# Kernel tuning notes

Measured on AMD Instinct MI355X. Metric: run time of the kernel, lower is better.

## Reference

```python
import jax, jax.numpy as jnp
import numpy as np

B, C, H, W = 2, 256, 64, 64
NUM_HEADS = 4
HEAD_DIM = C // NUM_HEADS
N = H * W


def setup_inputs() -> dict:
    key = jax.random.key(0)
    ks = jax.random.split(key, 10)
    x = jax.random.normal(ks[0], (B, C, H, W), dtype=jnp.float32)
    # mostly-True mask; diagonal forced True so every row has a valid key
    m = jax.random.uniform(ks[1], (B, N, N)) > 0.1
    spatial_mask = m | jnp.eye(N, dtype=bool)[None]
    s = 1.0 / np.sqrt(C)
    wq = jax.random.normal(ks[2], (C, C), dtype=jnp.float32) * s
    bq = jnp.zeros((C,), jnp.float32)
    wk = jax.random.normal(ks[3], (C, C), dtype=jnp.float32) * s
    bk = jnp.zeros((C,), jnp.float32)
    wv = jax.random.normal(ks[4], (C, C), dtype=jnp.float32) * s
    bv = jnp.zeros((C,), jnp.float32)
    # torch zero-inits out_proj; use random weights for a non-trivial baseline
    wo = jax.random.normal(ks[5], (C, C), dtype=jnp.float32) * s
    bo = jnp.zeros((C,), jnp.float32)
    return {"x": x, "spatial_mask": spatial_mask, "wq": wq, "bq": bq,
            "wk": wk, "bk": bk, "wv": wv, "bv": bv, "wo": wo, "bo": bo}


def reference(x, spatial_mask, wq, bq, wk, bk, wv, bv, wo, bo):
    b, c, h, w = x.shape
    n = h * w
    nh, hd = NUM_HEADS, HEAD_DIM
    scale = hd ** -0.5
    x_flat = x.reshape(b, c, n).transpose(0, 2, 1)           # [b, n, c]
    q = (x_flat @ wq.T + bq).reshape(b, n, nh, hd).transpose(0, 2, 1, 3)
    k = (x_flat @ wk.T + bk).reshape(b, n, nh, hd).transpose(0, 2, 1, 3)
    v = (x_flat @ wv.T + bv).reshape(b, n, nh, hd).transpose(0, 2, 1, 3)
    logits = jnp.einsum('bhqd,bhkd->bhqk', q, k) * scale      # [b, nh, n, n]
    logits = jnp.where(spatial_mask[:, None], logits, -jnp.inf)
    attn = jax.nn.softmax(logits, axis=-1)                    # dropout = identity (eval)
    out = jnp.einsum('bhqk,bhkd->bhqd', attn, v)              # [b, nh, n, hd]
    out = out.transpose(0, 2, 1, 3).reshape(b, n, c)
    out = out @ wo.T + bo
    return out.transpose(0, 2, 1).reshape(b, c, h, w)
```

## Files before the change

kernel.cpp:

```cpp
#include <hip/hip_runtime.h>
#include <math.h>

namespace {
constexpr int B_    = 2;
constexpr int C_    = 256;
constexpr int NHEAD = 4;
constexpr int HDIM  = 64;
constexpr int NTOK  = 4096;
constexpr float SCALE = 0.125f;
constexpr float LOG2E = 1.44269504f;
constexpr int QKV_BLOCKS = 3 * B_ * (NTOK / 64);
}

typedef _Float16 half8  __attribute__((ext_vector_type(8)));
typedef _Float16 half4  __attribute__((ext_vector_type(4)));
typedef __fp16   fp16x2 __attribute__((ext_vector_type(2)));
typedef float    floatx4 __attribute__((ext_vector_type(4)));
typedef int      int4v   __attribute__((ext_vector_type(4)));
typedef unsigned int uint2v __attribute__((ext_vector_type(2)));

__device__ __forceinline__ void plswap32(int &a, int &b) {
#if __has_builtin(__builtin_amdgcn_permlane32_swap)
    const uint2v r = __builtin_amdgcn_permlane32_swap((unsigned)a, (unsigned)b, false, false);
    a = (int)r[0]; b = (int)r[1];
#else
    asm volatile("s_nop 1\n\tv_permlane32_swap_b32 %0, %1\n\ts_nop 1"
                 : "+v"(a), "+v"(b));
#endif
}
__device__ __forceinline__ void plswap16(int &a, int &b) {
#if __has_builtin(__builtin_amdgcn_permlane16_swap)
    const uint2v r = __builtin_amdgcn_permlane16_swap((unsigned)a, (unsigned)b, false, false);
    a = (int)r[0]; b = (int)r[1];
#else
    asm volatile("s_nop 1\n\tv_permlane16_swap_b32 %0, %1\n\ts_nop 1"
                 : "+v"(a), "+v"(b));
#endif
}

__device__ __forceinline__ void gload_lds16(const _Float16* g, _Float16* l, int lane) {
#if __has_builtin(__builtin_amdgcn_global_load_lds)
    __builtin_amdgcn_global_load_lds(
        (const __attribute__((address_space(1))) void*)g,
        (__attribute__((address_space(3))) void*)l, 16, 0, 0);
#else
    *(half8*)((char*)l + lane * 16) = *(const half8*)g;
#endif
}

__device__ __forceinline__ half8 ldcvt8(const float* p) {
    const float4 a = *(const float4*)p;
    const float4 b = *(const float4*)(p + 4);
    half8 h;
    h[0]=(_Float16)a.x; h[1]=(_Float16)a.y; h[2]=(_Float16)a.z; h[3]=(_Float16)a.w;
    h[4]=(_Float16)b.x; h[5]=(_Float16)b.y; h[6]=(_Float16)b.z; h[7]=(_Float16)b.w;
    return h;
}

__global__ __launch_bounds__(256) void qkv_pack(
    const float* __restrict__ x,
    const float* __restrict__ wq, const float* __restrict__ wk,
    const float* __restrict__ wv,
    const float* __restrict__ bq, const float* __restrict__ bk,
    const float* __restrict__ bv,
    const unsigned int* __restrict__ m32, unsigned int* __restrict__ packed,
    _Float16* __restrict__ qo, _Float16* __restrict__ ko,
    _Float16* __restrict__ vo)
{
    if (blockIdx.x >= QKV_BLOCKS) {
        int c0 = 0, c1 = 0, c2 = 0, c3 = 0;
        #pragma unroll
        for (int i = 0; i < 16; i++) {
            const unsigned int d = m32[i];
            c0 += (d == 0x00000001u);
            c1 += (d == 0x3F803F80u);
            c2 += (d == 0x3F800000u);
            c3 += (d == 0x01010101u);
        }
        int fmt = 1, best = c1;
        if (c0 > best) { best = c0; fmt = 0; }
        if (c2 > best) { best = c2; fmt = 2; }
        if (c3 > best) { best = c3; fmt = 3; }

        const unsigned int W = (blockIdx.x - QKV_BLOCKS) * 256 + threadIdx.x;
        unsigned int bits = 0;
        if (fmt == 1) {
            const uint4* p4 = (const uint4*)(m32 + (size_t)W * 16);
            #pragma unroll
            for (int i = 0; i < 4; i++) {
                const uint4 v = p4[i];
                const unsigned int d[4] = { v.x, v.y, v.z, v.w };
                #pragma unroll
                for (int j = 0; j < 4; j++) {
                    const int e = i * 8 + j * 2;
                    bits |= ((d[j] & 0xFFFFu) ? 1u : 0u) << e;
                    bits |= ((d[j] >> 16)     ? 1u : 0u) << (e + 1);
                }
            }
        } else if (fmt != 3) {
            const uint4* p4 = (const uint4*)(m32 + (size_t)W * 32);
            #pragma unroll
            for (int i = 0; i < 8; i++) {
                const uint4 v = p4[i];
                bits |= (v.x ? 1u : 0u) << (i * 4 + 0);
                bits |= (v.y ? 1u : 0u) << (i * 4 + 1);
                bits |= (v.z ? 1u : 0u) << (i * 4 + 2);
                bits |= (v.w ? 1u : 0u) << (i * 4 + 3);
            }
        } else {
            const uint4* p4 = (const uint4*)(m32 + (size_t)W * 8);
            #pragma unroll
            for (int i = 0; i < 2; i++) {
                const uint4 v = p4[i];
                const unsigned int d[4] = { v.x, v.y, v.z, v.w };
                #pragma unroll
                for (int j = 0; j < 4; j++) {
                    const int e = (i * 4 + j) * 4;
                    bits |= ((d[j] & 0x000000FFu) ? 1u : 0u) << (e + 0);
                    bits |= ((d[j] & 0x0000FF00u) ? 1u : 0u) << (e + 1);
                    bits |= ((d[j] & 0x00FF0000u) ? 1u : 0u) << (e + 2);
                    bits |= ((d[j] & 0xFF000000u) ? 1u : 0u) << (e + 3);
                }
            }
        }
        packed[W] = bits;
        return;
    }

    const int bid = blockIdx.x;
    const int p   = bid >> 7;
    const int b   = (bid >> 6) & 1;
    const int nt  = bid & 63;

    const float* w    = (p == 0) ? wq : (p == 1) ? wk : wv;
    const float* bias = (p == 0) ? bq : (p == 1) ? bk : bv;

    const int t    = threadIdx.x;
    const int wid  = t >> 6;
    const int lane = t & 63;
    const int quad = lane >> 4;
    const int l15  = lane & 15;
    const int n0   = nt * 64;

    __shared__ _Float16 xsh[64 * 264];
    __shared__ _Float16 tbuf[64 * 72];

    const int srow = t >> 2;
    const int sc   = (t & 3) * 16;

    {
        const int cr = t >> 4;
        const int nu = (t & 15) * 4;
        const float* xb = x + (size_t)b * C_ * NTOK;
        #pragma unroll
        for (int cc = 0; cc < 16; cc++) {
            const int cl = cc * 16 + cr;
            const float4 v = *(const float4*)&xb[(size_t)cl * NTOK + n0 + nu];
            xsh[(nu + 0) * 264 + cl] = (_Float16)v.x;
            xsh[(nu + 1) * 264 + cl] = (_Float16)v.y;
            xsh[(nu + 2) * 264 + cl] = (_Float16)v.z;
            xsh[(nu + 3) * 264 + cl] = (_Float16)v.w;
        }
    }
    __syncthreads();

    const float* wrow = &w[(size_t)(wid * 16 + l15) * C_];

    for (int h = 0; h < NHEAD; h++) {
        const int co0 = h * 64;
        floatx4 acc[4];
        #pragma unroll
        for (int i = 0; i < 4; i++) acc[i] = (floatx4)0.f;

        #pragma unroll
        for (int c0 = 0; c0 < C_; c0 += 64) {
            const half8 a0 = ldcvt8(&wrow[(size_t)co0 * C_ + c0 + quad * 8]);
            const half8 a1 = ldcvt8(&wrow[(size_t)co0 * C_ + c0 + 32 + quad * 8]);
            #pragma unroll
            for (int nt2 = 0; nt2 < 4; nt2++) {
                const half8 b0 = *(const half8*)&xsh[(nt2 * 16 + l15) * 264 + c0 + quad * 8];
                const half8 b1 = *(const half8*)&xsh[(nt2 * 16 + l15) * 264 + c0 + 32 + quad * 8];
                acc[nt2] = __builtin_amdgcn_mfma_f32_16x16x32_f16(a0, b0, acc[nt2], 0, 0, 0);
                acc[nt2] = __builtin_amdgcn_mfma_f32_16x16x32_f16(a1, b1, acc[nt2], 0, 0, 0);
            }
        }

        const float4 bb4 = *(const float4*)&bias[co0 + wid * 16 + quad * 4];
        const float bb[4] = { bb4.x, bb4.y, bb4.z, bb4.w };

        if (p < 2) {
            const float osc = (p == 0) ? (SCALE * LOG2E) : 1.0f;
            #pragma unroll
            for (int nt2 = 0; nt2 < 4; nt2++) {
                half4 hv;
                #pragma unroll
                for (int i = 0; i < 4; i++)
                    hv[i] = (_Float16)((acc[nt2][i] + bb[i]) * osc);
                *(half4*)&tbuf[(nt2 * 16 + l15) * 72 + wid * 16 + quad * 4] = hv;
            }
            __syncthreads();
            _Float16* dh = (p == 0 ? qo : ko) + (size_t)(b * NHEAD + h) * NTOK * HDIM;
            const half8 o0 = *(const half8*)&tbuf[srow * 72 + sc];
            const half8 o1 = *(const half8*)&tbuf[srow * 72 + sc + 8];
            *(half8*)&dh[(size_t)(n0 + srow) * HDIM + sc]     = o0;
            *(half8*)&dh[(size_t)(n0 + srow) * HDIM + sc + 8] = o1;
        } else {
            #pragma unroll
            for (int nt2 = 0; nt2 < 4; nt2++)
                #pragma unroll
                for (int i = 0; i < 4; i++)
                    tbuf[(wid * 16 + quad * 4 + i) * 72 + nt2 * 16 + l15] =
                        (_Float16)(acc[nt2][i] + bb[i]);
            __syncthreads();
            _Float16* vth = vo + (size_t)(b * NHEAD + h) * HDIM * NTOK;
            const half8 o0 = *(const half8*)&tbuf[srow * 72 + sc];
            const half8 o1 = *(const half8*)&tbuf[srow * 72 + sc + 8];
            *(half8*)&vth[(size_t)srow * NTOK + n0 + sc]     = o0;
            *(half8*)&vth[(size_t)srow * NTOK + n0 + sc + 8] = o1;
        }
        __syncthreads();
    }
}

__global__ __launch_bounds__(512) void attn(
    const _Float16* __restrict__ q, const _Float16* __restrict__ k,
    const _Float16* __restrict__ vt, const unsigned int* __restrict__ mpacked,
    _Float16* __restrict__ ao)
{
    const int b  = blockIdx.z;
    const int h  = blockIdx.y;
    const int q0 = blockIdx.x * 128;
    const int t    = threadIdx.x;
    const int w    = t >> 6;
    const int lane = t & 63;
    const int quad = lane >> 4;
    const int l15  = lane & 15;
    const int half = w >> 2;
    const int w4   = w & 3;
    const int koff = half * (NTOK / 2);

    __shared__ __align__(16) char smem_raw[65536];
    _Float16* const sbase = (_Float16*)(smem_raw + half * 32768);

    const size_t head_off = (size_t)(b * NHEAD + h) * NTOK * HDIM;
    const _Float16* qb  = q  + head_off;
    const _Float16* kb  = k  + head_off;
    const _Float16* vtb = vt + head_off;
    const unsigned int* mrow = mpacked + (size_t)b * NTOK * 128;

    const int qrowa = q0 + w4 * 16 + l15;
    const int qrowb = qrowa + 64;
    const half8 aq0a = *(const half8*)&qb[(size_t)qrowa * HDIM + quad * 8];
    const half8 aq1a = *(const half8*)&qb[(size_t)qrowa * HDIM + 32 + quad * 8];
    const half8 aq0b = *(const half8*)&qb[(size_t)qrowb * HDIM + quad * 8];
    const half8 aq1b = *(const half8*)&qb[(size_t)qrowb * HDIM + 32 + quad * 8];
    const unsigned int* mqa = &mrow[(size_t)qrowa * 128];
    const unsigned int* mqb = &mrow[(size_t)qrowb * 128];

    const int jr  = l15 & 7;
    const int xs0 = (quad ^ jr) << 3;
    const int xs1 = ((quad + 4) ^ jr) << 3;

    uint2 mwa = *(const uint2*)&mqa[koff >> 5];
    uint2 mwb = *(const uint2*)&mqb[koff >> 5];
    uint2 mwa_nxt = mwa, mwb_nxt = mwb;

    float l_a = 0.f, l_b = 0.f;
    floatx4 oacca[4], oaccb[4];
    #pragma unroll
    for (int i = 0; i < 4; i++) { oacca[i] = (floatx4)0.f; oaccb[i] = (floatx4)0.f; }

#define STAGE(WO, K0N)                                                        \
    {                                                                         \
        const int rl = lane >> 3;                       \
        const int xc = ((lane & 7) ^ rl) << 3;        \
        const int c0 = w4 * 2, c1 = c0 + 1;                                   \
        gload_lds16(&kb[(size_t)((K0N) + c0 * 8 + rl) * HDIM + xc],           \
                    &sbase[(WO) + c0 * 512], lane);                           \
        gload_lds16(&kb[(size_t)((K0N) + c1 * 8 + rl) * HDIM + xc],           \
                    &sbase[(WO) + c1 * 512], lane);                           \
        gload_lds16(&vtb[(size_t)(c0 * 8 + rl) * NTOK + (K0N) + xc],          \
                    &sbase[(WO) + 4096 + c0 * 512], lane);                    \
        gload_lds16(&vtb[(size_t)(c1 * 8 + rl) * NTOK + (K0N) + xc],          \
                    &sbase[(WO) + 4096 + c1 * 512], lane);                    \
    }

    STAGE(0, koff)
    __syncthreads();

#define SOFTMAX_CT(SA, CT, WORD, SH, LL, Pa, Pb)                                  \
    {                                                                             \
        const unsigned nib = ((WORD) >> ((SH) + quad * 4)) & 0xFu;                \
        const float p0 = __builtin_amdgcn_exp2f((nib & 1u) ? SA[CT][0] : -3.0e38f);\
        const float p1 = __builtin_amdgcn_exp2f((nib & 2u) ? SA[CT][1] : -3.0e38f);\
        const float p2 = __builtin_amdgcn_exp2f((nib & 4u) ? SA[CT][2] : -3.0e38f);\
        const float p3 = __builtin_amdgcn_exp2f((nib & 8u) ? SA[CT][3] : -3.0e38f);\
        LL += (p0 + p1) + (p2 + p3);                                              \
        Pa = __builtin_bit_cast(int, __builtin_amdgcn_cvt_pkrtz(p0, p1));         \
        Pb = __builtin_bit_cast(int, __builtin_amdgcn_cvt_pkrtz(p2, p3));         \
    }

#define ATTN_TILE(RO, WO, KT, PF)                                                 \
    {                                                                             \
        if (PF) {                                                                 \
            const int k0n = koff + (KT) * 64 + 64;                                \
            STAGE(WO, k0n)                                                        \
            mwa_nxt = *(const uint2*)&mqa[k0n >> 5];                              \
            mwb_nxt = *(const uint2*)&mqb[k0n >> 5];                              \
        }                                                                         \
        floatx4 saa[4], sab[4];                                                   \
        __builtin_amdgcn_s_setprio(1);                                            \
        _Pragma("unroll")                                                         \
        for (int ct = 0; ct < 4; ct++) {                                          \
            saa[ct] = (floatx4)0.f; sab[ct] = (floatx4)0.f;                       \
            const half8 ka0 = *(const half8*)&sbase[(RO) + (ct*16 + l15)*64 + xs0];\
            const half8 ka1 = *(const half8*)&sbase[(RO) + (ct*16 + l15)*64 + xs1];\
            saa[ct] = __builtin_amdgcn_mfma_f32_16x16x32_f16(ka0, aq0a, saa[ct], 0, 0, 0); \
            saa[ct] = __builtin_amdgcn_mfma_f32_16x16x32_f16(ka1, aq1a, saa[ct], 0, 0, 0); \
            sab[ct] = __builtin_amdgcn_mfma_f32_16x16x32_f16(ka0, aq0b, sab[ct], 0, 0, 0); \
            sab[ct] = __builtin_amdgcn_mfma_f32_16x16x32_f16(ka1, aq1b, sab[ct], 0, 0, 0); \
        }                                                                         \
        __builtin_amdgcn_s_setprio(0);                                            \
        int A00,A01,A10,A11,A20,A21,A30,A31;                                      \
        int B00,B01,B10,B11,B20,B21,B30,B31;                                      \
        SOFTMAX_CT(saa, 0, mwa.x, 0,  l_a, A00, A01)                              \
        SOFTMAX_CT(saa, 1, mwa.x, 16, l_a, A10, A11)                              \
        SOFTMAX_CT(saa, 2, mwa.y, 0,  l_a, A20, A21)                              \
        SOFTMAX_CT(saa, 3, mwa.y, 16, l_a, A30, A31)                              \
        SOFTMAX_CT(sab, 0, mwb.x, 0,  l_b, B00, B01)                              \
        SOFTMAX_CT(sab, 1, mwb.x, 16, l_b, B10, B11)                              \
        SOFTMAX_CT(sab, 2, mwb.y, 0,  l_b, B20, B21)                              \
        SOFTMAX_CT(sab, 3, mwb.y, 16, l_b, B30, B31)                              \
        mwa = mwa_nxt; mwb = mwb_nxt;                                             \
        plswap32(A00, A10); plswap32(A01, A11);                                   \
        plswap32(A20, A30); plswap32(A21, A31);                                   \
        plswap16(A00, A10); plswap16(A01, A11);                                   \
        plswap16(A20, A30); plswap16(A21, A31);                                   \
        plswap32(B00, B10); plswap32(B01, B11);                                   \
        plswap32(B20, B30); plswap32(B21, B31);                                   \
        plswap16(B00, B10); plswap16(B01, B11);                                   \
        plswap16(B20, B30); plswap16(B21, B31);                                   \
        const half8 pb0a = __builtin_bit_cast(half8, (int4v){A00, A01, A10, A11});\
        const half8 pb1a = __builtin_bit_cast(half8, (int4v){A20, A21, A30, A31});\
        const half8 pb0b = __builtin_bit_cast(half8, (int4v){B00, B01, B10, B11});\
        const half8 pb1b = __builtin_bit_cast(half8, (int4v){B20, B21, B30, B31});\
        __builtin_amdgcn_s_setprio(1);                                            \
        _Pragma("unroll")                                                         \
        for (int dt = 0; dt < 4; dt++) {                                          \
            const half8 va0 = *(const half8*)&sbase[(RO) + 4096 + (dt*16 + l15)*64 + xs0];\
            const half8 va1 = *(const half8*)&sbase[(RO) + 4096 + (dt*16 + l15)*64 + xs1];\
            oacca[dt] = __builtin_amdgcn_mfma_f32_16x16x32_f16(va0, pb0a, oacca[dt], 0, 0, 0); \
            oacca[dt] = __builtin_amdgcn_mfma_f32_16x16x32_f16(va1, pb1a, oacca[dt], 0, 0, 0); \
            oaccb[dt] = __builtin_amdgcn_mfma_f32_16x16x32_f16(va0, pb0b, oaccb[dt], 0, 0, 0); \
            oaccb[dt] = __builtin_amdgcn_mfma_f32_16x16x32_f16(va1, pb1b, oaccb[dt], 0, 0, 0); \
        }                                                                         \
        __builtin_amdgcn_s_setprio(0);                                            \
        __syncthreads();                                                          \
    }

    for (int kt2 = 0; kt2 < 15; kt2++) {
        ATTN_TILE(0,    8192, 2 * kt2,     1)
        ATTN_TILE(8192, 0,    2 * kt2 + 1, 1)
    }
    ATTN_TILE(0,    8192, 30, 1)
    ATTN_TILE(8192, 0,    31, 0)

#undef ATTN_TILE
#undef SOFTMAX_CT
#undef STAGE

    l_a += __shfl_xor(l_a, 16, 64);
    l_a += __shfl_xor(l_a, 32, 64);
    l_b += __shfl_xor(l_b, 16, 64);
    l_b += __shfl_xor(l_b, 32, 64);

    __syncthreads();
    float* oex = (float*)smem_raw;
    float* lex = (float*)(smem_raw + 32768);
    if (w >= 4) {
        float* dst = &oex[((size_t)(w - 4) * 64 + lane) * 32];
        #pragma unroll
        for (int dt = 0; dt < 4; dt++) {
            *(floatx4*)&dst[dt * 4]      = oacca[dt];
            *(floatx4*)&dst[16 + dt * 4] = oaccb[dt];
        }
        if (quad == 0) {
            lex[(w - 4) * 16 + l15]      = l_a;
            lex[64 + (w - 4) * 16 + l15] = l_b;
        }
    }
    __syncthreads();
    if (w < 4) {
        const float* src = &oex[((size_t)w * 64 + lane) * 32];
        const float lta = l_a + lex[w * 16 + l15];
        const float ltb = l_b + lex[64 + w * 16 + l15];
        const float inva = (lta > 0.f) ? (1.0f / lta) : 0.f;
        const float invb = (ltb > 0.f) ? (1.0f / ltb) : 0.f;
        _Float16* aoba = ao + ((size_t)b * NTOK + q0 + w * 16 + l15) * C_ + h * 64;
        _Float16* aobb = ao + ((size_t)b * NTOK + q0 + 64 + w * 16 + l15) * C_ + h * 64;
        #pragma unroll
        for (int dt = 0; dt < 4; dt++) {
            const floatx4 o2a = *(const floatx4*)&src[dt * 4];
            const floatx4 o2b = *(const floatx4*)&src[16 + dt * 4];
            half4 ra, rb;
            #pragma unroll
            for (int rr = 0; rr < 4; rr++) {
                ra[rr] = (_Float16)((oacca[dt][rr] + o2a[rr]) * inva);
                rb[rr] = (_Float16)((oaccb[dt][rr] + o2b[rr]) * invb);
            }
            *(half4*)&aoba[dt * 16 + quad * 4] = ra;
            *(half4*)&aobb[dt * 16 + quad * 4] = rb;
        }
    }
}

__global__ __launch_bounds__(256) void out_mfma(
    const _Float16* __restrict__ ao, const float* __restrict__ wo,
    const float* __restrict__ bo, float* __restrict__ out)
{
    const int nt  = blockIdx.x;
    const int cot = blockIdx.y;
    const int b   = blockIdx.z;
    const int t    = threadIdx.x;
    const int wid  = t >> 6;
    const int lane = t & 63;
    const int quad = lane >> 4;
    const int l15  = lane & 15;
    const int n0  = nt * 64;
    const int co0 = cot * 64;

    __shared__ float tf[64 * 68];

    floatx4 acc[4];
    #pragma unroll
    for (int i = 0; i < 4; i++) acc[i] = (floatx4)0.f;

    const float* wrow = &wo[(size_t)(co0 + wid * 16 + l15) * C_];
    const _Float16* aob  = ao + ((size_t)b * NTOK + n0) * C_;

    #pragma unroll
    for (int c0 = 0; c0 < C_; c0 += 64) {
        const half8 a0 = ldcvt8(&wrow[c0 + quad * 8]);
        const half8 a1 = ldcvt8(&wrow[c0 + 32 + quad * 8]);
        #pragma unroll
        for (int nt2 = 0; nt2 < 4; nt2++) {
            const half8 b0 = *(const half8*)&aob[(size_t)(nt2 * 16 + l15) * C_ + c0 + quad * 8];
            const half8 b1 = *(const half8*)&aob[(size_t)(nt2 * 16 + l15) * C_ + c0 + 32 + quad * 8];
            acc[nt2] = __builtin_amdgcn_mfma_f32_16x16x32_f16(a0, b0, acc[nt2], 0, 0, 0);
            acc[nt2] = __builtin_amdgcn_mfma_f32_16x16x32_f16(a1, b1, acc[nt2], 0, 0, 0);
        }
    }

    #pragma unroll
    for (int nt2 = 0; nt2 < 4; nt2++)
        #pragma unroll
        for (int i = 0; i < 4; i++)
            tf[(wid * 16 + quad * 4 + i) * 68 + nt2 * 16 + l15] = acc[nt2][i];
    __syncthreads();

    const int row = t >> 2;
    const int c4  = (t & 3) * 16;
    const float bb = bo[co0 + row];
    float* orow = &out[((size_t)(b * C_ + co0 + row)) * NTOK + n0 + c4];
    #pragma unroll
    for (int u = 0; u < 4; u++) {
        float4 v = *(const float4*)&tf[row * 68 + c4 + u * 4];
        v.x += bb; v.y += bb; v.z += bb; v.w += bb;
        *(float4*)&orow[u * 4] = v;
    }
}

extern "C" void kernel_launch(void* const* d_in, const int* in_sizes, int n_in,
                              void* d_out, int out_size, void* d_ws, size_t ws_size,
                              hipStream_t stream) {
    const float* x    = (const float*)d_in[0];
    const void*  mask = d_in[1];
    const float* wq   = (const float*)d_in[2];
    const float* bq   = (const float*)d_in[3];
    const float* wk   = (const float*)d_in[4];
    const float* bk   = (const float*)d_in[5];
    const float* wv   = (const float*)d_in[6];
    const float* bv   = (const float*)d_in[7];
    const float* wo   = (const float*)d_in[8];
    const float* bo   = (const float*)d_in[9];
    float* out = (float*)d_out;

    const size_t qkv_elems = (size_t)B_ * NHEAD * NTOK * HDIM;
    _Float16* wsh = (_Float16*)d_ws;
    _Float16* qbuf  = wsh;
    _Float16* kbuf  = wsh + qkv_elems;
    _Float16* vtbuf = wsh + 2 * qkv_elems;
    _Float16* aobuf = wsh + 3 * qkv_elems;
    unsigned int* mpacked = (unsigned int*)(wsh + 4 * qkv_elems);

    qkv_pack<<<dim3(QKV_BLOCKS + (B_ * NTOK * 128) / 256), 256, 0, stream>>>(
        x, wq, wk, wv, bq, bk, bv,
        (const unsigned int*)mask, mpacked, qbuf, kbuf, vtbuf);
    attn<<<dim3(NTOK / 128, NHEAD, B_), 512, 0, stream>>>(
        qbuf, kbuf, vtbuf, mpacked, aobuf);
    out_mfma<<<dim3(NTOK / 64, C_ / 64, B_), 256, 0, stream>>>(
        aobuf, wo, bo, out);
}
```

Before: 284.2 us.

## Triple-buffer K/V tiles in LDS with two-tile-ahead prefetch and partial vmcnt waits

Grows the per-half LDS ring from two to three K/V tile buffers and prefetches K/V tiles and mask words two tiles ahead instead of one. The full __syncthreads at the end of each tile becomes an explicit s_waitcnt vmcnt(6) plus s_barrier, so only the older tile's loads must have landed. The loop is unrolled by three to rotate the buffers. The goal is to hide global-to-LDS latency better. In exchange, LDS use rises from 64KB to 96KB per block, which likely drops co-resident blocks per CU from two to one.

```diff
diff --git a/kernel.cpp b/kernel.cpp
--- a/kernel.cpp
+++ b/kernel.cpp
@@ -239,8 +239,8 @@
     const int w4   = w & 3;
     const int koff = half * (NTOK / 2);
 
-    __shared__ __align__(16) char smem_raw[65536];
-    _Float16* const sbase = (_Float16*)(smem_raw + half * 32768);
+    __shared__ __align__(16) char smem_raw[98304];
+    _Float16* const sbase = (_Float16*)(smem_raw + half * 49152);
 
     const size_t head_off = (size_t)(b * NHEAD + h) * NTOK * HDIM;
     const _Float16* qb  = q  + head_off;
@@ -260,10 +260,6 @@
     const int jr  = l15 & 7;
     const int xs0 = (quad ^ jr) << 3;
     const int xs1 = ((quad + 4) ^ jr) << 3;
-
-    uint2 mwa = *(const uint2*)&mqa[koff >> 5];
-    uint2 mwb = *(const uint2*)&mqb[koff >> 5];
-    uint2 mwa_nxt = mwa, mwb_nxt = mwb;
 
     float l_a = 0.f, l_b = 0.f;
     floatx4 oacca[4], oaccb[4];
@@ -285,8 +281,16 @@
                     &sbase[(WO) + 4096 + c1 * 512], lane);                    \
     }
 
+    uint2 mwa  = *(const uint2*)&mqa[(koff) >> 5];
+    uint2 mwb  = *(const uint2*)&mqb[(koff) >> 5];
+    uint2 mwa1 = *(const uint2*)&mqa[(koff + 64) >> 5];
+    uint2 mwb1 = *(const uint2*)&mqb[(koff + 64) >> 5];
+    uint2 mwa2 = mwa1, mwb2 = mwb1;
+
     STAGE(0, koff)
-    __syncthreads();
+    STAGE(8192, koff + 64)
+    asm volatile("s_waitcnt vmcnt(6)" ::: "memory");
+    __builtin_amdgcn_s_barrier();
 
 #define SOFTMAX_CT(SA, CT, WORD, SH, LL, Pa, Pb)                                  \
     {                                                                             \
@@ -300,13 +304,13 @@
         Pb = __builtin_bit_cast(int, __builtin_amdgcn_cvt_pkrtz(p2, p3));         \
     }
 
-#define ATTN_TILE(RO, WO, KT, PF)                                                 \
+#define ATTN_TILE(RO, WO, KT, PF, VMS)                                            \
     {                                                                             \
         if (PF) {                                                                 \
-            const int k0n = koff + (KT) * 64 + 64;                                \
+            const int k0n = koff + (KT) * 64 + 128;                 \
             STAGE(WO, k0n)                                                        \
-            mwa_nxt = *(const uint2*)&mqa[k0n >> 5];                              \
-            mwb_nxt = *(const uint2*)&mqb[k0n >> 5];                              \
+            mwa2 = *(const uint2*)&mqa[k0n >> 5];                                 \
+            mwb2 = *(const uint2*)&mqb[k0n >> 5];                                 \
         }                                                                         \
         floatx4 saa[4], sab[4];                                                   \
         __builtin_amdgcn_s_setprio(1);                                            \
@@ -331,7 +335,7 @@
         SOFTMAX_CT(sab, 1, mwb.x, 16, l_b, B10, B11)                              \
         SOFTMAX_CT(sab, 2, mwb.y, 0,  l_b, B20, B21)                              \
         SOFTMAX_CT(sab, 3, mwb.y, 16, l_b, B30, B31)                              \
-        mwa = mwa_nxt; mwb = mwb_nxt;                                             \
+        mwa = mwa1; mwb = mwb1; mwa1 = mwa2; mwb1 = mwb2;                         \
         plswap32(A00, A10); plswap32(A01, A11);                                   \
         plswap32(A20, A30); plswap32(A21, A31);                                   \
         plswap16(A00, A10); plswap16(A01, A11);                                   \
@@ -355,15 +359,17 @@
             oaccb[dt] = __builtin_amdgcn_mfma_f32_16x16x32_f16(va1, pb1b, oaccb[dt], 0, 0, 0); \
         }                                                                         \
         __builtin_amdgcn_s_setprio(0);                                            \
-        __syncthreads();                                                          \
-    }
-
-    for (int kt2 = 0; kt2 < 15; kt2++) {
-        ATTN_TILE(0,    8192, 2 * kt2,     1)
-        ATTN_TILE(8192, 0,    2 * kt2 + 1, 1)
-    }
-    ATTN_TILE(0,    8192, 30, 1)
-    ATTN_TILE(8192, 0,    31, 0)
+        asm volatile("s_waitcnt vmcnt(" VMS ")" ::: "memory");                    \
+        __builtin_amdgcn_s_barrier();                                             \
+    }
+
+    for (int kt3 = 0; kt3 < 10; kt3++) {
+        ATTN_TILE(0,     16384, 3 * kt3,     1, "6")
+        ATTN_TILE(8192,  0,     3 * kt3 + 1, 1, "6")
+        ATTN_TILE(16384, 8192,  3 * kt3 + 2, 1, "6")
+    }
+    ATTN_TILE(0,    16384, 30, 0, "0")
+    ATTN_TILE(8192, 0,     31, 0, "0")
 
 #undef ATTN_TILE
 #undef SOFTMAX_CT
```

New measurement: 290.9 us. +2.4%, slower.
